# Optimization experiments

Hardware: AMD Instinct MI355X
Metric: run time of the kernel (lower is better)

Reference implementation:

```python
import jax, jax.numpy as jnp
import numpy as np

N_POINTS = 1048576
N_CLUSTERS = 16384
D_FEAT = 64


def setup_inputs() -> dict:
    key = jax.random.key(0)
    ks = jax.random.split(key, 6)
    features = jax.random.normal(ks[0], (N_CLUSTERS, D_FEAT), dtype=jnp.float32)
    labels = jax.random.randint(ks[1], (N_POINTS,), 0, N_CLUSTERS, dtype=jnp.int32)
    cluster_centers = jax.random.normal(ks[2], (N_CLUSTERS, 3), dtype=jnp.float32)
    points = jax.random.normal(ks[3], (N_POINTS, 3), dtype=jnp.float32)
    # Glorot-uniform like Keras Dense defaults
    lim1 = np.sqrt(6.0 / (D_FEAT + 3 + 128)).astype(np.float32)
    lim2 = np.sqrt(6.0 / (128 + 64)).astype(np.float32)
    W1 = jax.random.uniform(ks[4], (D_FEAT + 3, 128), minval=-lim1, maxval=lim1, dtype=jnp.float32)
    b1 = jnp.zeros((128,), dtype=jnp.float32)
    W2 = jax.random.uniform(ks[5], (128, 64), minval=-lim2, maxval=lim2, dtype=jnp.float32)
    b2 = jnp.zeros((64,), dtype=jnp.float32)
    return {"features": features, "labels": labels, "cluster_centers": cluster_centers,
            "points": points, "W1": W1, "b1": b1, "W2": W2, "b2": b2}


def reference(features, labels, cluster_centers, points, W1, b1, W2, b2):
    center_features = features[labels]                 # [N, D_FEAT] gather
    point_center_coords = cluster_centers[labels]      # [N, 3] gather
    x = jnp.concatenate([center_features, point_center_coords - points], axis=-1)  # [N, 67]
    h = jax.nn.relu(x @ W1 + b1)                       # [N, 128]
    out = jax.nn.relu(h @ W2 + b2)                     # [N, 64]
    return out
```

## Files before the change

kernel.cpp:

```cpp
#include <hip/hip_runtime.h>
#include <hip/hip_bf16.h>

#define NPTS 1048576
#define NCLU 16384
#define DF   64
#define H1   128
#define H2   64
#define BP   64
#define NBLK 1024
#define ITERS (NPTS / (BP * NBLK))
#define K1P  104
#define K2P  136

typedef __bf16 bf16x8 __attribute__((ext_vector_type(8)));
typedef float  f32x4  __attribute__((ext_vector_type(4)));
typedef unsigned short u16x4 __attribute__((ext_vector_type(4)));
typedef unsigned short u16x8 __attribute__((ext_vector_type(8)));

__device__ __forceinline__ unsigned short f2b(float f) {
  unsigned v; __builtin_memcpy(&v, &f, 4);
  v += 0x7fffu + ((v >> 16) & 1u);
  return (unsigned short)(v >> 16);
}

__global__ __launch_bounds__(256, 4)
void cvt_feat(const float* __restrict__ f, unsigned short* __restrict__ o) {
  int i = (blockIdx.x * 256 + threadIdx.x) * 4;
  f32x4 v = *(const f32x4*)&f[i];
  u16x4 h;
  #pragma unroll
  for (int j = 0; j < 4; ++j) h[j] = f2b(v[j]);
  *(u16x4*)&o[i] = h;
}

__global__ __launch_bounds__(256, 2)
void fused_gather_mlp(const float* __restrict__ feat,
                      const int* __restrict__ labels,
                      const float* __restrict__ centers,
                      const float* __restrict__ points,
                      const float* __restrict__ W1,
                      const float* __restrict__ b1,
                      const float* __restrict__ W2,
                      const float* __restrict__ b2,
                      float* __restrict__ out,
                      const unsigned short* __restrict__ featbf,
                      int use_bf)
{
  __shared__ __align__(16) unsigned short sX[BP][K1P];
  __shared__ __align__(16) unsigned short sW1[H1][K1P];
  __shared__ __align__(16) unsigned short sH[BP][K2P];
  __shared__ __align__(16) unsigned short sW2[H2][K2P];
  __shared__ __align__(16) float sB1[H1];

  const int t    = threadIdx.x;
  const int w    = t >> 6;
  const int lane = t & 63;
  const int quad = lane >> 4, l16 = lane & 15;
  const int m0   = w * 16;

  if (t < 32) *(f32x4*)&sB1[t * 4] = *(const f32x4*)&b1[t * 4];

  #pragma unroll
  for (int i = 0; i < 6; ++i) {
    int task = t + 256 * i;
    int n = task & 127, kc = task >> 7;
    u16x8 h;
    #pragma unroll
    for (int j = 0; j < 8; ++j) {
      int k = kc * 8 + j;
      float v = (k < 67) ? W1[k * H1 + n] : 0.f;
      h[j] = f2b(v);
    }
    *(u16x8*)&sW1[n][kc * 8] = h;
  }
  #pragma unroll
  for (int i = 0; i < 4; ++i) {
    int task = t + 256 * i;
    int n = task & 63, kc = task >> 6;
    u16x8 h;
    #pragma unroll
    for (int j = 0; j < 8; ++j) h[j] = f2b(W2[(kc * 8 + j) * H2 + n]);
    *(u16x8*)&sW2[n][kc * 8] = h;
  }
  if (lane < 48) {
    int r = lane & 15, c = 9 + (lane >> 4);
    u16x8 z = {0, 0, 0, 0, 0, 0, 0, 0};
    *(u16x8*)&sX[m0 + r][c * 8] = z;
  }

  f32x4 bias2v[4];
  #pragma unroll
  for (int nt2 = 0; nt2 < 4; ++nt2)
    bias2v[nt2] = *(const f32x4*)&b2[nt2 * 16 + quad * 4];

  __syncthreads();

  float bias1[8];
  #pragma unroll
  for (int nt = 0; nt < 8; ++nt) bias1[nt] = sB1[nt * 16 + l16];

  for (int it = 0; it < ITERS; ++it) {
    const int p0 = (blockIdx.x * ITERS + it) * BP;

    #pragma unroll
    for (int i = 0; i < 2; ++i) {
      int task = lane + 64 * i;
      int row = task >> 3, kc = task & 7;
      int lab = labels[p0 + m0 + row];
      if (use_bf) {
        *(u16x8*)&sX[m0 + row][kc * 8] = *(const u16x8*)&featbf[lab * DF + kc * 8];
      } else {
        f32x4 v0 = *(const f32x4*)&feat[lab * DF + kc * 8];
        f32x4 v1 = *(const f32x4*)&feat[lab * DF + kc * 8 + 4];
        u16x8 h;
        #pragma unroll
        for (int j = 0; j < 4; ++j) { h[j] = f2b(v0[j]); h[j + 4] = f2b(v1[j]); }
        *(u16x8*)&sX[m0 + row][kc * 8] = h;
      }
    }
    if (lane < 16) {
      int row = lane, p = p0 + m0 + row;
      int lab = labels[p];
      u16x8 h = {0, 0, 0, 0, 0, 0, 0, 0};
      #pragma unroll
      for (int j = 0; j < 3; ++j) h[j] = f2b(centers[lab * 3 + j] - points[p * 3 + j]);
      *(u16x8*)&sX[m0 + row][DF] = h;
    }

    f32x4 acc[8];
    #pragma unroll
    for (int i = 0; i < 8; ++i) acc[i] = (f32x4){0.f, 0.f, 0.f, 0.f};
    #pragma unroll
    for (int ks = 0; ks < 3; ++ks) {
      int k0 = ks * 32 + quad * 8;
      bf16x8 a = *(const bf16x8*)&sX[m0 + l16][k0];
      #pragma unroll
      for (int nt = 0; nt < 8; ++nt) {
        bf16x8 b = *(const bf16x8*)&sW1[nt * 16 + l16][k0];
        acc[nt] = __builtin_amdgcn_mfma_f32_16x16x32_bf16(a, b, acc[nt], 0, 0, 0);
      }
    }
    #pragma unroll
    for (int nt = 0; nt < 8; ++nt) {
      int n = nt * 16 + l16;
      #pragma unroll
      for (int r = 0; r < 4; ++r) {
        float v = acc[nt][r] + bias1[nt];
        v = v > 0.f ? v : 0.f;
        sH[m0 + quad * 4 + r][n] = f2b(v);
      }
    }

    f32x4 acc2[4];
    #pragma unroll
    for (int i = 0; i < 4; ++i) acc2[i] = bias2v[i];
    #pragma unroll
    for (int ks = 0; ks < 4; ++ks) {
      int k0 = ks * 32 + quad * 8;
      bf16x8 hf = *(const bf16x8*)&sH[m0 + l16][k0];
      #pragma unroll
      for (int nt2 = 0; nt2 < 4; ++nt2) {
        bf16x8 wf = *(const bf16x8*)&sW2[nt2 * 16 + l16][k0];
        acc2[nt2] = __builtin_amdgcn_mfma_f32_16x16x32_bf16(wf, hf, acc2[nt2], 0, 0, 0);
      }
    }
    const long prow = (long)(p0 + m0 + l16) * H2;
    #pragma unroll
    for (int nt2 = 0; nt2 < 4; ++nt2) {
      f32x4 v = acc2[nt2];
      #pragma unroll
      for (int r = 0; r < 4; ++r) v[r] = v[r] > 0.f ? v[r] : 0.f;
      *(f32x4*)&out[prow + nt2 * 16 + quad * 4] = v;
    }
  }
}

extern "C" void kernel_launch(void* const* d_in, const int* in_sizes, int n_in,
                              void* d_out, int out_size, void* d_ws, size_t ws_size,
                              hipStream_t stream) {
  const float* feat   = (const float*)d_in[0];
  const int*   labels = (const int*)d_in[1];
  const float* cen    = (const float*)d_in[2];
  const float* pts    = (const float*)d_in[3];
  const float* W1     = (const float*)d_in[4];
  const float* b1     = (const float*)d_in[5];
  const float* W2     = (const float*)d_in[6];
  const float* b2     = (const float*)d_in[7];
  float*       outp   = (float*)d_out;

  const size_t featbf_bytes = (size_t)NCLU * DF * sizeof(unsigned short);
  int use_bf = (ws_size >= featbf_bytes) ? 1 : 0;
  unsigned short* featbf = (unsigned short*)d_ws;

  if (use_bf)
    cvt_feat<<<dim3(NCLU * DF / (256 * 4)), dim3(256), 0, stream>>>(feat, featbf);

  fused_gather_mlp<<<dim3(NBLK), dim3(256), 0, stream>>>(
      feat, labels, cen, pts, W1, b1, W2, b2, outp, featbf, use_bf);
}
```

Measured before the change: 385.6 us.

## Software-pipeline label and feature gathers one iteration ahead of the MLP compute

Restructures the per-iteration loop so the gathered feature rows and coordinate deltas for the next tile are loaded into registers while the current tile's MFMAs run. Labels are prefetched two iterations ahead. The goal is to hide the latency of dependent global gathers behind compute in this memory-bound kernel. It costs extra registers, which may lower occupancy, and adds redundant loads at the final iteration.

After: 351.5 us (median of 2 runs). 8.8% less time.

```diff
diff --git a/kernel.cpp b/kernel.cpp
--- a/kernel.cpp
+++ b/kernel.cpp
@@ -57,6 +57,9 @@
   const int lane = t & 63;
   const int quad = lane >> 4, l16 = lane & 15;
   const int m0   = w * 16;
+  const int rowA = lane >> 3;
+  const int rowB = rowA + 8;
+  const int kc8  = (lane & 7) * 8;
 
   if (t < 32) *(f32x4*)&sB1[t * 4] = *(const f32x4*)&b1[t * 4];
 
@@ -99,33 +102,70 @@
   #pragma unroll
   for (int nt = 0; nt < 8; ++nt) bias1[nt] = sB1[nt * 16 + l16];
 
+  const int base = blockIdx.x * ITERS;
+
+  u16x8 gA, gB, hD = {0, 0, 0, 0, 0, 0, 0, 0};
+  {
+    int labA0 = labels[base * BP + m0 + rowA];
+    int labB0 = labels[base * BP + m0 + rowB];
+    if (use_bf) {
+      gA = *(const u16x8*)&featbf[labA0 * DF + kc8];
+      gB = *(const u16x8*)&featbf[labB0 * DF + kc8];
+    } else {
+      f32x4 a0 = *(const f32x4*)&feat[labA0 * DF + kc8];
+      f32x4 a1 = *(const f32x4*)&feat[labA0 * DF + kc8 + 4];
+      f32x4 b0 = *(const f32x4*)&feat[labB0 * DF + kc8];
+      f32x4 b1v = *(const f32x4*)&feat[labB0 * DF + kc8 + 4];
+      #pragma unroll
+      for (int j = 0; j < 4; ++j) {
+        gA[j] = f2b(a0[j]); gA[j + 4] = f2b(a1[j]);
+        gB[j] = f2b(b0[j]); gB[j + 4] = f2b(b1v[j]);
+      }
+    }
+    if (lane < 16) {
+      int p = base * BP + m0 + lane;
+      int labD0 = labels[p];
+      #pragma unroll
+      for (int j = 0; j < 3; ++j) hD[j] = f2b(centers[labD0 * 3 + j] - points[(long)p * 3 + j]);
+    }
+  }
+  const int tl1 = (ITERS > 1) ? 1 : 0;
+  int labA1 = labels[(base + tl1) * BP + m0 + rowA];
+  int labB1 = labels[(base + tl1) * BP + m0 + rowB];
+  int labD1 = (lane < 16) ? labels[(base + tl1) * BP + m0 + lane] : 0;
+
   for (int it = 0; it < ITERS; ++it) {
-    const int p0 = (blockIdx.x * ITERS + it) * BP;
-
-    #pragma unroll
-    for (int i = 0; i < 2; ++i) {
-      int task = lane + 64 * i;
-      int row = task >> 3, kc = task & 7;
-      int lab = labels[p0 + m0 + row];
-      if (use_bf) {
-        *(u16x8*)&sX[m0 + row][kc * 8] = *(const u16x8*)&featbf[lab * DF + kc * 8];
-      } else {
-        f32x4 v0 = *(const f32x4*)&feat[lab * DF + kc * 8];
-        f32x4 v1 = *(const f32x4*)&feat[lab * DF + kc * 8 + 4];
-        u16x8 h;
-        #pragma unroll
-        for (int j = 0; j < 4; ++j) { h[j] = f2b(v0[j]); h[j + 4] = f2b(v1[j]); }
-        *(u16x8*)&sX[m0 + row][kc * 8] = h;
+    const int p0 = (base + it) * BP;
+
+    *(u16x8*)&sX[m0 + rowA][kc8] = gA;
+    *(u16x8*)&sX[m0 + rowB][kc8] = gB;
+    if (lane < 16) *(u16x8*)&sX[m0 + lane][DF] = hD;
+
+    const int tn = (it + 1 < ITERS) ? it + 1 : it;
+    u16x8 gA1, gB1, hD1 = {0, 0, 0, 0, 0, 0, 0, 0};
+    if (use_bf) {
+      gA1 = *(const u16x8*)&featbf[labA1 * DF + kc8];
+      gB1 = *(const u16x8*)&featbf[labB1 * DF + kc8];
+    } else {
+      f32x4 a0 = *(const f32x4*)&feat[labA1 * DF + kc8];
+      f32x4 a1 = *(const f32x4*)&feat[labA1 * DF + kc8 + 4];
+      f32x4 b0 = *(const f32x4*)&feat[labB1 * DF + kc8];
+      f32x4 b1v = *(const f32x4*)&feat[labB1 * DF + kc8 + 4];
+      #pragma unroll
+      for (int j = 0; j < 4; ++j) {
+        gA1[j] = f2b(a0[j]); gA1[j + 4] = f2b(a1[j]);
+        gB1[j] = f2b(b0[j]); gB1[j + 4] = f2b(b1v[j]);
       }
     }
     if (lane < 16) {
-      int row = lane, p = p0 + m0 + row;
-      int lab = labels[p];
-      u16x8 h = {0, 0, 0, 0, 0, 0, 0, 0};
-      #pragma unroll
-      for (int j = 0; j < 3; ++j) h[j] = f2b(centers[lab * 3 + j] - points[p * 3 + j]);
-      *(u16x8*)&sX[m0 + row][DF] = h;
-    }
+      int pn = (base + tn) * BP + m0 + lane;
+      #pragma unroll
+      for (int j = 0; j < 3; ++j) hD1[j] = f2b(centers[labD1 * 3 + j] - points[(long)pn * 3 + j]);
+    }
+    const int t2 = (it + 2 < ITERS) ? it + 2 : ITERS - 1;
+    int labA2 = labels[(base + t2) * BP + m0 + rowA];
+    int labB2 = labels[(base + t2) * BP + m0 + rowB];
+    int labD2 = (lane < 16) ? labels[(base + t2) * BP + m0 + lane] : 0;
 
     f32x4 acc[8];
     #pragma unroll
@@ -172,6 +212,9 @@
       for (int r = 0; r < 4; ++r) v[r] = v[r] > 0.f ? v[r] : 0.f;
       *(f32x4*)&out[prow + nt2 * 16 + quad * 4] = v;
     }
+
+    gA = gA1; gB = gB1; hD = hD1;
+    labA1 = labA2; labB1 = labB2; labD1 = labD2;
   }
 }
 
```

## Software-pipeline label and feature gathers two iterations ahead in registers

Applied to the files above, without the earlier changes.

Restructures the per-block loop into a two-stage register prefetch pipeline. Labels are loaded four iterations ahead and the gathered bf16 feature rows and center offsets two iterations ahead, held in registers, then written to shared memory at the start of each iteration. This hides the dependent label-then-feature gather latency behind the MFMA work of the current tile. In exchange it raises register pressure and keeps a redundant clamped prefetch at the tail.

Result: faster. 363.1 us (-5.8%).

```diff
diff --git a/kernel.cpp b/kernel.cpp
--- a/kernel.cpp
+++ b/kernel.cpp
@@ -31,6 +31,43 @@
   #pragma unroll
   for (int j = 0; j < 4; ++j) h[j] = f2b(v[j]);
   *(u16x4*)&o[i] = h;
+}
+
+__device__ __forceinline__ void load_labels(const int* __restrict__ labels, int off,
+                                            int lane, int rowA, int rowB,
+                                            int& lA, int& lB, int& lD) {
+  lA = labels[off + rowA];
+  lB = labels[off + rowB];
+  lD = (lane < 16) ? labels[off + lane] : 0;
+}
+
+__device__ __forceinline__ void load_payload(const unsigned short* __restrict__ featbf,
+                                             const float* __restrict__ feat,
+                                             const float* __restrict__ centers,
+                                             const float* __restrict__ points,
+                                             int use_bf, int lane, int kc8, int rowOff,
+                                             int lA, int lB, int lD,
+                                             u16x8& gA, u16x8& gB, u16x8& hD) {
+  if (use_bf) {
+    gA = *(const u16x8*)&featbf[lA * DF + kc8];
+    gB = *(const u16x8*)&featbf[lB * DF + kc8];
+  } else {
+    f32x4 a0 = *(const f32x4*)&feat[lA * DF + kc8];
+    f32x4 a1 = *(const f32x4*)&feat[lA * DF + kc8 + 4];
+    f32x4 b0 = *(const f32x4*)&feat[lB * DF + kc8];
+    f32x4 b1x = *(const f32x4*)&feat[lB * DF + kc8 + 4];
+    #pragma unroll
+    for (int j = 0; j < 4; ++j) {
+      gA[j] = f2b(a0[j]); gA[j + 4] = f2b(a1[j]);
+      gB[j] = f2b(b0[j]); gB[j + 4] = f2b(b1x[j]);
+    }
+  }
+  hD = (u16x8){0, 0, 0, 0, 0, 0, 0, 0};
+  if (lane < 16) {
+    long p = rowOff + lane;
+    #pragma unroll
+    for (int j = 0; j < 3; ++j) hD[j] = f2b(centers[lD * 3 + j] - points[p * 3 + j]);
+  }
 }
 
 __global__ __launch_bounds__(256, 2)
@@ -57,6 +94,9 @@
   const int lane = t & 63;
   const int quad = lane >> 4, l16 = lane & 15;
   const int m0   = w * 16;
+  const int rowA = lane >> 3;
+  const int rowB = rowA + 8;
+  const int kc8  = (lane & 7) * 8;
 
   if (t < 32) *(f32x4*)&sB1[t * 4] = *(const f32x4*)&b1[t * 4];
 
@@ -99,78 +139,140 @@
   #pragma unroll
   for (int nt = 0; nt < 8; ++nt) bias1[nt] = sB1[nt * 16 + l16];
 
-  for (int it = 0; it < ITERS; ++it) {
-    const int p0 = (blockIdx.x * ITERS + it) * BP;
-
-    #pragma unroll
-    for (int i = 0; i < 2; ++i) {
-      int task = lane + 64 * i;
-      int row = task >> 3, kc = task & 7;
-      int lab = labels[p0 + m0 + row];
-      if (use_bf) {
-        *(u16x8*)&sX[m0 + row][kc * 8] = *(const u16x8*)&featbf[lab * DF + kc * 8];
-      } else {
-        f32x4 v0 = *(const f32x4*)&feat[lab * DF + kc * 8];
-        f32x4 v1 = *(const f32x4*)&feat[lab * DF + kc * 8 + 4];
-        u16x8 h;
-        #pragma unroll
-        for (int j = 0; j < 4; ++j) { h[j] = f2b(v0[j]); h[j + 4] = f2b(v1[j]); }
-        *(u16x8*)&sX[m0 + row][kc * 8] = h;
+  const int base = blockIdx.x * ITERS;
+
+  u16x8 gXa, gXb, hXd;
+  u16x8 gYa, gYb, hYd;
+  int lPa, lPb, lPd;
+  int lQa, lQb, lQd;
+  {
+    int la, lb, ld;
+    load_labels(labels, base * BP + m0, lane, rowA, rowB, la, lb, ld);
+    load_payload(featbf, feat, centers, points, use_bf, lane, kc8,
+                 base * BP + m0, la, lb, ld, gXa, gXb, hXd);
+    int i1 = (1 < ITERS) ? 1 : ITERS - 1;
+    load_labels(labels, (base + i1) * BP + m0, lane, rowA, rowB, la, lb, ld);
+    load_payload(featbf, feat, centers, points, use_bf, lane, kc8,
+                 (base + i1) * BP + m0, la, lb, ld, gYa, gYb, hYd);
+    int i2 = (2 < ITERS) ? 2 : ITERS - 1;
+    int i3 = (3 < ITERS) ? 3 : ITERS - 1;
+    load_labels(labels, (base + i2) * BP + m0, lane, rowA, rowB, lPa, lPb, lPd);
+    load_labels(labels, (base + i3) * BP + m0, lane, rowA, rowB, lQa, lQb, lQd);
+  }
+
+  for (int it = 0; it < ITERS; it += 2) {
+    {
+      const int p0 = (base + it) * BP;
+      *(u16x8*)&sX[m0 + rowA][kc8] = gXa;
+      *(u16x8*)&sX[m0 + rowB][kc8] = gXb;
+      if (lane < 16) *(u16x8*)&sX[m0 + lane][DF] = hXd;
+      const int i2 = (it + 2 < ITERS) ? it + 2 : ITERS - 1;
+      load_payload(featbf, feat, centers, points, use_bf, lane, kc8,
+                   (base + i2) * BP + m0, lPa, lPb, lPd, gXa, gXb, hXd);
+      const int i4 = (it + 4 < ITERS) ? it + 4 : ITERS - 1;
+      load_labels(labels, (base + i4) * BP + m0, lane, rowA, rowB, lPa, lPb, lPd);
+
+      f32x4 acc[8];
+      #pragma unroll
+      for (int i = 0; i < 8; ++i) acc[i] = (f32x4){0.f, 0.f, 0.f, 0.f};
+      #pragma unroll
+      for (int ks = 0; ks < 3; ++ks) {
+        int k0 = ks * 32 + quad * 8;
+        bf16x8 a = *(const bf16x8*)&sX[m0 + l16][k0];
+        #pragma unroll
+        for (int nt = 0; nt < 8; ++nt) {
+          bf16x8 b = *(const bf16x8*)&sW1[nt * 16 + l16][k0];
+          acc[nt] = __builtin_amdgcn_mfma_f32_16x16x32_bf16(a, b, acc[nt], 0, 0, 0);
+        }
+      }
+      #pragma unroll
+      for (int nt = 0; nt < 8; ++nt) {
+        int n = nt * 16 + l16;
+        #pragma unroll
+        for (int r = 0; r < 4; ++r) {
+          float v = acc[nt][r] + bias1[nt];
+          v = v > 0.f ? v : 0.f;
+          sH[m0 + quad * 4 + r][n] = f2b(v);
+        }
+      }
+      f32x4 acc2[4];
+      #pragma unroll
+      for (int i = 0; i < 4; ++i) acc2[i] = bias2v[i];
+      #pragma unroll
+      for (int ks = 0; ks < 4; ++ks) {
+        int k0 = ks * 32 + quad * 8;
+        bf16x8 hf = *(const bf16x8*)&sH[m0 + l16][k0];
+        #pragma unroll
+        for (int nt2 = 0; nt2 < 4; ++nt2) {
+          bf16x8 wf = *(const bf16x8*)&sW2[nt2 * 16 + l16][k0];
+          acc2[nt2] = __builtin_amdgcn_mfma_f32_16x16x32_bf16(wf, hf, acc2[nt2], 0, 0, 0);
+        }
+      }
+      const long prow = (long)(p0 + m0 + l16) * H2;
+      #pragma unroll
+      for (int nt2 = 0; nt2 < 4; ++nt2) {
+        f32x4 v = acc2[nt2];
+        #pragma unroll
+        for (int r = 0; r < 4; ++r) v[r] = v[r] > 0.f ? v[r] : 0.f;
+        *(f32x4*)&out[prow + nt2 * 16 + quad * 4] = v;
       }
     }
-    if (lane < 16) {
-      int row = lane, p = p0 + m0 + row;
-      int lab = labels[p];
-      u16x8 h = {0, 0, 0, 0, 0, 0, 0, 0};
-      #pragma unroll
-      for (int j = 0; j < 3; ++j) h[j] = f2b(centers[lab * 3 + j] - points[p * 3 + j]);
-      *(u16x8*)&sX[m0 + row][DF] = h;
-    }
-
-    f32x4 acc[8];
-    #pragma unroll
-    for (int i = 0; i < 8; ++i) acc[i] = (f32x4){0.f, 0.f, 0.f, 0.f};
-    #pragma unroll
-    for (int ks = 0; ks < 3; ++ks) {
-      int k0 = ks * 32 + quad * 8;
-      bf16x8 a = *(const bf16x8*)&sX[m0 + l16][k0];
+
+    {
+      const int p0 = (base + it + 1) * BP;
+      *(u16x8*)&sX[m0 + rowA][kc8] = gYa;
+      *(u16x8*)&sX[m0 + rowB][kc8] = gYb;
+      if (lane < 16) *(u16x8*)&sX[m0 + lane][DF] = hYd;
+      const int i3 = (it + 3 < ITERS) ? it + 3 : ITERS - 1;
+      load_payload(featbf, feat, centers, points, use_bf, lane, kc8,
+                   (base + i3) * BP + m0, lQa, lQb, lQd, gYa, gYb, hYd);
+      const int i5 = (it + 5 < ITERS) ? it + 5 : ITERS - 1;
+      load_labels(labels, (base + i5) * BP + m0, lane, rowA, rowB, lQa, lQb, lQd);
+
+      f32x4 acc[8];
+      #pragma unroll
+      for (int i = 0; i < 8; ++i) acc[i] = (f32x4){0.f, 0.f, 0.f, 0.f};
+      #pragma unroll
+      for (int ks = 0; ks < 3; ++ks) {
+        int k0 = ks * 32 + quad * 8;
+        bf16x8 a = *(const bf16x8*)&sX[m0 + l16][k0];
+        #pragma unroll
+        for (int nt = 0; nt < 8; ++nt) {
+          bf16x8 b = *(const bf16x8*)&sW1[nt * 16 + l16][k0];
+          acc[nt] = __builtin_amdgcn_mfma_f32_16x16x32_bf16(a, b, acc[nt], 0, 0, 0);
+        }
+      }
       #pragma unroll
       for (int nt = 0; nt < 8; ++nt) {
-        bf16x8 b = *(const bf16x8*)&sW1[nt * 16 + l16][k0];
-        acc[nt] = __builtin_amdgcn_mfma_f32_16x16x32_bf16(a, b, acc[nt], 0, 0, 0);
-      }
-    }
-    #pragma unroll
-    for (int nt = 0; nt < 8; ++nt) {
-      int n = nt * 16 + l16;
-      #pragma unroll
-      for (int r = 0; r < 4; ++r) {
-        float v = acc[nt][r] + bias1[nt];
-        v = v > 0.f ? v : 0.f;
-        sH[m0 + quad * 4 + r][n] = f2b(v);
-      }
-    }
-
-    f32x4 acc2[4];
-    #pragma unroll
-    for (int i = 0; i < 4; ++i) acc2[i] = bias2v[i];
-    #pragma unroll
-    for (int ks = 0; ks < 4; ++ks) {
-      int k0 = ks * 32 + quad * 8;
-      bf16x8 hf = *(const bf16x8*)&sH[m0 + l16][k0];
+        int n = nt * 16 + l16;
+        #pragma unroll
+        for (int r = 0; r < 4; ++r) {
+          float v = acc[nt][r] + bias1[nt];
+          v = v > 0.f ? v : 0.f;
+          sH[m0 + quad * 4 + r][n] = f2b(v);
+        }
+      }
+      f32x4 acc2[4];
+      #pragma unroll
+      for (int i = 0; i < 4; ++i) acc2[i] = bias2v[i];
+      #pragma unroll
+      for (int ks = 0; ks < 4; ++ks) {
+        int k0 = ks * 32 + quad * 8;
+        bf16x8 hf = *(const bf16x8*)&sH[m0 + l16][k0];
+        #pragma unroll
+        for (int nt2 = 0; nt2 < 4; ++nt2) {
+          bf16x8 wf = *(const bf16x8*)&sW2[nt2 * 16 + l16][k0];
+          acc2[nt2] = __builtin_amdgcn_mfma_f32_16x16x32_bf16(wf, hf, acc2[nt2], 0, 0, 0);
+        }
+      }
+      const long prow = (long)(p0 + m0 + l16) * H2;
       #pragma unroll
       for (int nt2 = 0; nt2 < 4; ++nt2) {
-        bf16x8 wf = *(const bf16x8*)&sW2[nt2 * 16 + l16][k0];
-        acc2[nt2] = __builtin_amdgcn_mfma_f32_16x16x32_bf16(wf, hf, acc2[nt2], 0, 0, 0);
-      }
-    }
-    const long prow = (long)(p0 + m0 + l16) * H2;
-    #pragma unroll
-    for (int nt2 = 0; nt2 < 4; ++nt2) {
-      f32x4 v = acc2[nt2];
-      #pragma unroll
-      for (int r = 0; r < 4; ++r) v[r] = v[r] > 0.f ? v[r] : 0.f;
-      *(f32x4*)&out[prow + nt2 * 16 + quad * 4] = v;
+        f32x4 v = acc2[nt2];
+        #pragma unroll
+        for (int r = 0; r < 4; ++r) v[r] = v[r] > 0.f ? v[r] : 0.f;
+        *(f32x4*)&out[prow + nt2 * 16 + quad * 4] = v;
+      }
     }
   }
 }
```
